# Optimization experiments

Measured on AMD Instinct MI355X. Metric: run time of the kernel, lower is better.

The kernel has to match this reference:

```python
import jax, jax.numpy as jnp
import numpy as np
import math

INPUT_SIZE = 1024
HIDDEN_SIZE = 1024
BATCH = 4096


def setup_inputs() -> dict:
    key = jax.random.key(0)
    ks = jax.random.split(key, 16)
    stddev = 1.0 / math.sqrt(HIDDEN_SIZE)

    def unif(k, shape):
        return jax.random.uniform(k, shape, minval=-stddev, maxval=stddev, dtype=jnp.float32)

    inp = {
        'x': jax.random.normal(ks[0], (BATCH, INPUT_SIZE), dtype=jnp.float32),
        'h_prev': jax.random.normal(ks[1], (BATCH, HIDDEN_SIZE), dtype=jnp.float32),
        'c_prev': jax.random.normal(ks[2], (BATCH, HIDDEN_SIZE), dtype=jnp.float32),
        'igx': unif(ks[3], (INPUT_SIZE, HIDDEN_SIZE)),
        'igu': unif(ks[4], (HIDDEN_SIZE, HIDDEN_SIZE)),
        'ib': unif(ks[5], (HIDDEN_SIZE,)),
        'fgx': unif(ks[6], (INPUT_SIZE, HIDDEN_SIZE)),
        'fgu': unif(ks[7], (HIDDEN_SIZE, HIDDEN_SIZE)),
        'fb': unif(ks[8], (HIDDEN_SIZE,)),
        'ogx': unif(ks[9], (INPUT_SIZE, HIDDEN_SIZE)),
        'ogu': unif(ks[10], (HIDDEN_SIZE, HIDDEN_SIZE)),
        'ob': unif(ks[11], (HIDDEN_SIZE,)),
        'cgx': unif(ks[12], (INPUT_SIZE, HIDDEN_SIZE)),
        'cgu': unif(ks[13], (HIDDEN_SIZE, HIDDEN_SIZE)),
        'cb': unif(ks[14], (HIDDEN_SIZE,)),
    }
    return inp


def reference(x, h_prev, c_prev, igx, igu, ib, fgx, fgu, fb, ogx, ogu, ob, cgx, cgu, cb):
    # Fuse the 8 gate matmuls into 2 GEMMs via concatenated weights.
    # Wx: [input_size, 4H], Wh: [hidden, 4H], b: [4H]; gate order i,f,o,c.
    Wx = jnp.concatenate([igx, fgx, ogx, cgx], axis=1)
    Wh = jnp.concatenate([igu, fgu, ogu, cgu], axis=1)
    b = jnp.concatenate([ib, fb, ob, cb], axis=0)
    gates = x @ Wx + h_prev @ Wh + b  # [B, 4H]
    H = c_prev.shape[-1]
    ig = jax.nn.sigmoid(gates[:, 0 * H:1 * H])
    fg = jax.nn.sigmoid(gates[:, 1 * H:2 * H])
    og = jax.nn.sigmoid(gates[:, 2 * H:3 * H])
    cc = jnp.tanh(gates[:, 3 * H:4 * H])
    c = fg * c_prev + ig * cc
    h = og * jnp.tanh(c)
    return (h, c)
```

## Files before the change

### kernel.cpp

```cpp
#include <hip/hip_runtime.h>
#include <hip/hip_bf16.h>

typedef unsigned short u16;
typedef unsigned int u32;
typedef short bf16x8 __attribute__((ext_vector_type(8)));
typedef float f32x4 __attribute__((ext_vector_type(4)));
typedef u16 u16x8 __attribute__((ext_vector_type(8)));

#define HID 1024
#define BATCH 4096
#define KTOT 2048

__device__ __forceinline__ u16 f2bf(float f) {
  u32 v = __builtin_bit_cast(u32, f);
  u32 r = (v + 0x7fffu + ((v >> 16) & 1u)) >> 16;
  return (u16)r;
}
__device__ __forceinline__ float sigmoid_fast(float x) {
  return 1.0f / (1.0f + __expf(-x));
}
__device__ __forceinline__ float tanh_fast(float x) {
  return 2.0f * sigmoid_fast(2.0f * x) - 1.0f;
}
__device__ __forceinline__ void gl_lds16(const void* g, void* l) {
  __builtin_amdgcn_global_load_lds(
      (const __attribute__((address_space(1))) u32*)g,
      (__attribute__((address_space(3))) u32*)l, 16, 0, 0);
}

__global__ __launch_bounds__(256) void prep_xh(
    const float* __restrict__ x, const float* __restrict__ hp,
    u16* __restrict__ xh) {
  int c = blockIdx.x * 256 + threadIdx.x;
  int row = c >> 8;
  int col0 = (c & 255) << 3;
  const float* src = (col0 < 1024) ? (x + (size_t)row * 1024 + col0)
                                   : (hp + (size_t)row * 1024 + (col0 - 1024));
  f32x4 a = *(const f32x4*)(src);
  f32x4 b = *(const f32x4*)(src + 4);
  u16x8 v;
#pragma unroll
  for (int j = 0; j < 4; ++j) { v[j] = f2bf(a[j]); v[j + 4] = f2bf(b[j]); }
  *(u16x8*)(xh + (size_t)row * KTOT + col0) = v;
}

__global__ __launch_bounds__(256) void prep_w(
    const float* __restrict__ igx, const float* __restrict__ fgx,
    const float* __restrict__ ogx, const float* __restrict__ cgx,
    const float* __restrict__ igu, const float* __restrict__ fgu,
    const float* __restrict__ ogu, const float* __restrict__ cgu,
    u16* __restrict__ bt) {
  const float* srcs[8] = {igx, fgx, ogx, cgx, igu, fgu, ogu, cgu};
  int bid = blockIdx.x;
  int m = bid >> 8;
  int tile = bid & 255;
  int th = tile & 15, tk = tile >> 4;
  int h0 = th << 6, k0 = tk << 6;
  int g = m & 3, which = m >> 2;
  const float* W = srcs[m];

  int t = threadIdx.x;
  int hl = t & 63, cc = t >> 6;
  int h = h0 + hl;
  int np = ((h >> 4) << 6) + (g << 4) + (h & 15);
  size_t dst_row = (size_t)np * KTOT + (size_t)which * 1024;

#pragma unroll
  for (int ci = 0; ci < 2; ++ci) {
    int c = cc + ci * 4;
    int kb = k0 + (c << 3);
    u16x8 v;
#pragma unroll
    for (int j = 0; j < 8; ++j) v[j] = f2bf(W[(size_t)(kb + j) * HID + h]);
    *(u16x8*)(&bt[dst_row + kb]) = v;
  }
}

__global__ __launch_bounds__(256) void lstm_gemm(
    const u16* __restrict__ xh, const u16* __restrict__ bt,
    const float* __restrict__ cprev,
    const float* __restrict__ ib, const float* __restrict__ fb,
    const float* __restrict__ ob, const float* __restrict__ cb,
    float* __restrict__ hout, float* __restrict__ cout) {
  __shared__ u16 As[128 * 32];
  __shared__ u16 Bs[128 * 32];

  int t = threadIdx.x;
  int brow = blockIdx.x, bcol = blockIdx.y;
  int w = t >> 6, l = t & 63;
  int wr = (w >> 1) * 64, wc = (w & 1) * 64;
  int lrow = l & 15, quad = l >> 4;

  f32x4 acc[4][4] = {};

  int ar0 = t >> 2;
  int asub = (t & 3) * 8;
  int grow = brow * 128;
  size_t brow_b = (size_t)(bcol * 128);

  for (int kt = 0; kt < 64; ++kt) {
    __syncthreads();
    int kk = kt * 32;
    gl_lds16(xh + (size_t)(grow + ar0) * KTOT + kk + asub, &As[t * 8]);
    gl_lds16(xh + (size_t)(grow + ar0 + 64) * KTOT + kk + asub, &As[(t + 256) * 8]);
    gl_lds16(bt + (brow_b + ar0) * KTOT + kk + asub, &Bs[t * 8]);
    gl_lds16(bt + (brow_b + ar0 + 64) * KTOT + kk + asub, &Bs[(t + 256) * 8]);
    __syncthreads();

    bf16x8 af[4], bfr[4];
#pragma unroll
    for (int i = 0; i < 4; ++i) {
      af[i]  = *(const bf16x8*)&As[(wr + i * 16 + lrow) * 32 + quad * 8];
      bfr[i] = *(const bf16x8*)&Bs[(wc + i * 16 + lrow) * 32 + quad * 8];
    }
#pragma unroll
    for (int mi = 0; mi < 4; ++mi)
#pragma unroll
      for (int ni = 0; ni < 4; ++ni)
        acc[mi][ni] = __builtin_amdgcn_mfma_f32_16x16x32_bf16(
            af[mi], bfr[ni], acc[mi][ni], 0, 0, 0);
  }

  int sb = bcol * 2 + (w & 1);
  int hcol = sb * 16 + lrow;
  float bi = ib[hcol];
  float bff = fb[hcol];
  float bo = ob[hcol];
  float bc = cb[hcol];

#pragma unroll
  for (int mi = 0; mi < 4; ++mi) {
    int row0 = grow + wr + mi * 16 + quad * 4;
#pragma unroll
    for (int r = 0; r < 4; ++r) {
      size_t idx = (size_t)(row0 + r) * HID + hcol;
      float gi = sigmoid_fast(acc[mi][0][r] + bi);
      float gf = sigmoid_fast(acc[mi][1][r] + bff);
      float go = sigmoid_fast(acc[mi][2][r] + bo);
      float gc = tanh_fast(acc[mi][3][r] + bc);
      float cp = cprev[idx];
      float cv = gf * cp + gi * gc;
      float hv = go * tanh_fast(cv);
      hout[idx] = hv;
      cout[idx] = cv;
    }
  }
}

extern "C" void kernel_launch(void* const* d_in, const int* in_sizes, int n_in,
                              void* d_out, int out_size, void* d_ws, size_t ws_size,
                              hipStream_t stream) {
  const float* x   = (const float*)d_in[0];
  const float* hp  = (const float*)d_in[1];
  const float* cp  = (const float*)d_in[2];
  const float* igx = (const float*)d_in[3];
  const float* igu = (const float*)d_in[4];
  const float* ib  = (const float*)d_in[5];
  const float* fgx = (const float*)d_in[6];
  const float* fgu = (const float*)d_in[7];
  const float* fb  = (const float*)d_in[8];
  const float* ogx = (const float*)d_in[9];
  const float* ogu = (const float*)d_in[10];
  const float* ob  = (const float*)d_in[11];
  const float* cgx = (const float*)d_in[12];
  const float* cgu = (const float*)d_in[13];
  const float* cb  = (const float*)d_in[14];

  u16* bt = (u16*)d_ws;
  u16* xh = bt + (size_t)4096 * 2048;
  float* hout = (float*)d_out;
  float* cout = hout + (size_t)BATCH * HID;

  prep_xh<<<4096, 256, 0, stream>>>(x, hp, xh);
  prep_w<<<2048, 256, 0, stream>>>(igx, fgx, ogx, cgx, igu, fgu, ogu, cgu, bt);
  lstm_gemm<<<dim3(32, 32), 256, 0, stream>>>(xh, bt, cp, ib, fb, ob, cb,
                                              hout, cout);
}
```

Measured before the change: 244.4 us.

## Transpose weights through LDS and swizzle GEMM LDS tiles to avoid bank conflicts

The weight-prep kernel now reads fp32 weight tiles with coalesced vector loads, converts them to bf16 into a padded LDS tile, and writes the transposed rows as contiguous 16-byte chunks. This replaces strided scalar global reads. The GEMM permutes the 16-byte chunk within each LDS row using an XOR of row bits, with matching reads on the fragment side, to cut LDS bank conflicts. It adds an LDS pass and a barrier to the prep kernel.

```diff
diff --git a/kernel.cpp b/kernel.cpp
--- a/kernel.cpp
+++ b/kernel.cpp
@@ -50,6 +50,7 @@
     const float* __restrict__ igu, const float* __restrict__ fgu,
     const float* __restrict__ ogu, const float* __restrict__ cgu,
     u16* __restrict__ bt) {
+  __shared__ u16 lds[64 * 66];
   const float* srcs[8] = {igx, fgx, ogx, cgx, igu, fgu, ogu, cgu};
   int bid = blockIdx.x;
   int m = bid >> 8;
@@ -57,23 +58,36 @@
   int th = tile & 15, tk = tile >> 4;
   int h0 = th << 6, k0 = tk << 6;
   int g = m & 3, which = m >> 2;
-  const float* W = srcs[m];
+  const float* W = srcs[m] + (size_t)k0 * HID + h0;
 
   int t = threadIdx.x;
-  int hl = t & 63, cc = t >> 6;
-  int h = h0 + hl;
-  int np = ((h >> 4) << 6) + (g << 4) + (h & 15);
-  size_t dst_row = (size_t)np * KTOT + (size_t)which * 1024;
 
+  int r1 = t >> 4;
+  int c1 = (t & 15) << 2;
 #pragma unroll
-  for (int ci = 0; ci < 2; ++ci) {
-    int c = cc + ci * 4;
-    int kb = k0 + (c << 3);
-    u16x8 v;
+  for (int p = 0; p < 4; ++p) {
+    int row = (p << 4) + r1;
+    f32x4 v = *(const f32x4*)(W + (size_t)row * HID + c1);
+    u32 p0 = (u32)f2bf(v[0]) | ((u32)f2bf(v[1]) << 16);
+    u32 p1 = (u32)f2bf(v[2]) | ((u32)f2bf(v[3]) << 16);
+    u32* d = (u32*)&lds[row * 66 + c1];
+    d[0] = p0;
+    d[1] = p1;
+  }
+  __syncthreads();
+
+  int nl = t >> 2;
+  int kc = t & 3;
+  int row_np = ((h0 >> 4) << 6) + ((nl >> 4) << 6) + (g << 4) + (nl & 15);
+  size_t dst = (size_t)row_np * KTOT + (size_t)which * 1024 + k0;
+  u16x8 a, b;
 #pragma unroll
-    for (int j = 0; j < 8; ++j) v[j] = f2bf(W[(size_t)(kb + j) * HID + h]);
-    *(u16x8*)(&bt[dst_row + kb]) = v;
+  for (int j = 0; j < 8; ++j) {
+    a[j] = lds[(kc * 8 + j) * 66 + nl];
+    b[j] = lds[(kc * 8 + 32 + j) * 66 + nl];
   }
+  *(u16x8*)(&bt[dst + kc * 8]) = a;
+  *(u16x8*)(&bt[dst + kc * 8 + 32]) = b;
 }
 
 __global__ __launch_bounds__(256) void lstm_gemm(
@@ -93,25 +107,26 @@
 
   f32x4 acc[4][4] = {};
 
-  int ar0 = t >> 2;
-  int asub = (t & 3) * 8;
+  int srow = t >> 2;
+  int schunk = ((t & 3) ^ ((t >> 3) & 3)) << 3;
+  int quadp = ((quad ^ ((lrow >> 1) & 3)) << 3);
   int grow = brow * 128;
   size_t brow_b = (size_t)(bcol * 128);
 
   for (int kt = 0; kt < 64; ++kt) {
     __syncthreads();
     int kk = kt * 32;
-    gl_lds16(xh + (size_t)(grow + ar0) * KTOT + kk + asub, &As[t * 8]);
-    gl_lds16(xh + (size_t)(grow + ar0 + 64) * KTOT + kk + asub, &As[(t + 256) * 8]);
-    gl_lds16(bt + (brow_b + ar0) * KTOT + kk + asub, &Bs[t * 8]);
-    gl_lds16(bt + (brow_b + ar0 + 64) * KTOT + kk + asub, &Bs[(t + 256) * 8]);
+    gl_lds16(xh + (size_t)(grow + srow) * KTOT + kk + schunk, &As[t * 8]);
+    gl_lds16(xh + (size_t)(grow + srow + 64) * KTOT + kk + schunk, &As[(t + 256) * 8]);
+    gl_lds16(bt + (brow_b + srow) * KTOT + kk + schunk, &Bs[t * 8]);
+    gl_lds16(bt + (brow_b + srow + 64) * KTOT + kk + schunk, &Bs[(t + 256) * 8]);
     __syncthreads();
 
     bf16x8 af[4], bfr[4];
 #pragma unroll
     for (int i = 0; i < 4; ++i) {
-      af[i]  = *(const bf16x8*)&As[(wr + i * 16 + lrow) * 32 + quad * 8];
-      bfr[i] = *(const bf16x8*)&Bs[(wc + i * 16 + lrow) * 32 + quad * 8];
+      af[i]  = *(const bf16x8*)&As[(wr + i * 16 + lrow) * 32 + quadp];
+      bfr[i] = *(const bf16x8*)&Bs[(wc + i * 16 + lrow) * 32 + quadp];
     }
 #pragma unroll
     for (int mi = 0; mi < 4; ++mi)
```

Result: faster. 234.6 us (-4.0%).
